# Kernel optimization log

Measured on AMD Instinct MI355X. Metric: run time of the kernel, lower is better.

Reference implementation:

```python
import jax, jax.numpy as jnp
import numpy as np

IN_DIM = 512
REDUCED = IN_DIM // 8  # reduction_ratio = 8
B, C, H, W = 8, 32, 64, IN_DIM


def setup_inputs() -> dict:
    key = jax.random.key(0)
    ks = jax.random.split(key, 9)
    s_in = 1.0 / np.sqrt(IN_DIM)
    inp = {
        "x": jax.random.normal(ks[0], (B, C, H, W), dtype=jnp.float32),
        # torch Linear weights stored here as [in, out] for y = x @ w + b
        "wq": jax.random.uniform(ks[1], (IN_DIM, REDUCED), jnp.float32, -s_in, s_in),
        "bq": jax.random.uniform(ks[2], (REDUCED,), jnp.float32, -s_in, s_in),
        "wk": jax.random.uniform(ks[3], (IN_DIM, REDUCED), jnp.float32, -s_in, s_in),
        "bk": jax.random.uniform(ks[4], (REDUCED,), jnp.float32, -s_in, s_in),
        "wv": jax.random.uniform(ks[5], (IN_DIM, IN_DIM), jnp.float32, -s_in, s_in),
        "bv": jax.random.uniform(ks[6], (IN_DIM,), jnp.float32, -s_in, s_in),
        "wo": jax.random.uniform(ks[7], (IN_DIM, IN_DIM), jnp.float32, -s_in, s_in),
        "bo": jax.random.uniform(ks[8], (IN_DIM,), jnp.float32, -s_in, s_in),
    }
    return inp


def reference(x, wq, bq, wk, bk, wv, bv, wo, bo):
    b, c, h, w = x.shape
    n = c * h  # attention tokens = flattened C*H positions, feature dim = W
    q = (x @ wq + bq).reshape(b, n, REDUCED)   # [B, N, r]
    k = (x @ wk + bk).reshape(b, n, REDUCED)   # [B, N, r]
    v = (x @ wv + bv).reshape(b, n, w)         # [B, N, W]
    energy = jnp.einsum("bnr,bmr->bnm", q, k)  # [B, N, N]
    attn = jax.nn.softmax(energy, axis=-1)
    out = jnp.einsum("bnm,bmd->bnd", attn, v).reshape(b, c, h, w)
    out = out @ wo + bo
    return out + x
```

## Files before the change

### kernel.cpp

```cpp
#include <hip/hip_runtime.h>

typedef __bf16 bf16x8 __attribute__((ext_vector_type(8)));
typedef float  f32x4  __attribute__((ext_vector_type(4)));

union U8 { uint4 v; unsigned short u[8]; };

static __device__ __forceinline__ float bf2f(unsigned short u) {
    union { unsigned int i; float f; } c; c.i = ((unsigned int)u) << 16; return c.f;
}
static __device__ __forceinline__ unsigned short f2bf(float f) {
    union { float f; unsigned int i; } c; c.f = f;
    unsigned int x = c.i;
    unsigned int r = (x + 0x7FFFu + ((x >> 16) & 1u)) >> 16;
    return (unsigned short)r;
}

static __device__ __forceinline__ U8 load8(const float* p) {
    U8 r;
    const float4 a = *(const float4*)p;
    const float4 b = *(const float4*)(p + 4);
    r.u[0] = f2bf(a.x); r.u[1] = f2bf(a.y); r.u[2] = f2bf(a.z); r.u[3] = f2bf(a.w);
    r.u[4] = f2bf(b.x); r.u[5] = f2bf(b.y); r.u[6] = f2bf(b.z); r.u[7] = f2bf(b.w);
    return r;
}

static __device__ __forceinline__ void gld_lds16(const void* g, void* l) {
    __builtin_amdgcn_global_load_lds(
        (const __attribute__((address_space(1))) unsigned int*)g,
        (__attribute__((address_space(3))) unsigned int*)l, 16, 0, 0);
}

__global__ __launch_bounds__(256)
void pack(const float* __restrict__ x, unsigned short* __restrict__ xb,
          const float* __restrict__ bq, const float* __restrict__ bk,
          const float* __restrict__ bv, float* __restrict__ ball,
          const float* __restrict__ wv, const float* __restrict__ wo,
          const float* __restrict__ wq, const float* __restrict__ wk,
          unsigned short* __restrict__ wAllT, unsigned short* __restrict__ woT)
{
    const int bid = blockIdx.x, t = threadIdx.x;
    if (bid < 2048) {
        const long i = ((long)bid * 256 + t) * 16;
        U8 a = load8(x + i);
        U8 b = load8(x + i + 8);
        *(uint4*)(xb + i) = a.v;
        *(uint4*)(xb + i + 8) = b.v;
        if (bid == 0) {
            ball[t]       = t < 64 ? bq[t] : (t < 128 ? bk[t - 64] : bv[t - 128]);
            ball[t + 256] = bv[t + 128];
            if (t < 128) ball[t + 512] = bv[t + 384];
        }
        return;
    }
    __shared__ float sT[64][65];
    const int b2 = bid - 2048;
    const int zz = b2 >> 6, rem = b2 & 63;
    const int cx = rem & 7, ry = rem >> 3;
    const float* src; unsigned short* dst; int C;
    if      (zz == 0) { src = wv; dst = wAllT + 128 * 512; C = 512; }
    else if (zz == 1) { src = wo; dst = woT;               C = 512; }
    else if (zz == 2) { src = wq; dst = wAllT;             C = 64;  }
    else              { src = wk; dst = wAllT + 64 * 512;  C = 64;  }
    const int R = 512;
    const int c0 = cx * 64, r0 = ry * 64;
    if (c0 >= C) return;
    #pragma unroll
    for (int k = 0; k < 16; ++k) {
        const int lin = k * 256 + t;
        const int i = lin >> 6, j = lin & 63;
        sT[i][j] = src[(long)(r0 + i) * C + c0 + j];
    }
    __syncthreads();
    #pragma unroll
    for (int k = 0; k < 16; ++k) {
        const int lin = k * 256 + t;
        const int o = lin >> 6, i2 = lin & 63;
        dst[(long)(c0 + o) * R + r0 + i2] = f2bf(sT[i2][o]);
    }
}

template<bool BIAS, bool RES, bool OUT_F32, bool TRANSC, bool MIXED>
__global__ __launch_bounds__(256, 4)
void gemm128(const unsigned short* __restrict__ A, int lda,
             const unsigned short* __restrict__ B, int ldb,
             void* __restrict__ Cp, int ldc,
             void* __restrict__ Cp2,
             const float* __restrict__ bias,
             const float* __restrict__ resid,
             int K)
{
    __shared__ __align__(16) unsigned short sA[128 * 64];
    __shared__ __align__(16) unsigned short sB[128 * 64];

    const int t = threadIdx.x, wave = t >> 6, lane = t & 63;
    const int lr = lane & 15, quad = lane >> 4;
    const int rowBase = blockIdx.y * 128, colBase = blockIdx.x * 128;
    const int wm = (wave >> 1) * 64, wn = (wave & 1) * 64;

    const int srow  = lane >> 3;
    const int sslot = lane & 7;

    f32x4 acc[4][4];
    #pragma unroll
    for (int mt = 0; mt < 4; ++mt)
        #pragma unroll
        for (int nt = 0; nt < 4; ++nt) acc[mt][nt] = (f32x4){0.f, 0.f, 0.f, 0.f};

    for (int kt = 0; kt < K; kt += 64) {
        #pragma unroll
        for (int is = 0; is < 4; ++is) {
            const int r0  = wave * 32 + is * 8;
            const int row = r0 + srow;
            const int swz = (sslot ^ (row & 7)) << 4;
            gld_lds16((const char*)A + ((long)(rowBase + row) * lda + kt) * 2 + swz,
                      (char*)sA + r0 * 128);
            gld_lds16((const char*)B + ((long)(colBase + row) * ldb + kt) * 2 + swz,
                      (char*)sB + r0 * 128);
        }
        __syncthreads();

        #pragma unroll
        for (int ks = 0; ks < 2; ++ks) {
            const int kb = ks * 64 + quad * 16;
            bf16x8 bfr[4];
            #pragma unroll
            for (int nt = 0; nt < 4; ++nt) {
                const int row = wn + nt * 16 + lr;
                bfr[nt] = *(const bf16x8*)((const char*)sB + row * 128 + (kb ^ ((row & 7) << 4)));
            }
            #pragma unroll
            for (int mt = 0; mt < 4; ++mt) {
                const int row = wm + mt * 16 + lr;
                bf16x8 af = *(const bf16x8*)((const char*)sA + row * 128 + (kb ^ ((row & 7) << 4)));
                #pragma unroll
                for (int nt = 0; nt < 4; ++nt)
                    acc[mt][nt] = __builtin_amdgcn_mfma_f32_16x16x32_bf16(af, bfr[nt], acc[mt][nt], 0, 0, 0);
            }
        }
        __syncthreads();
    }

    float* Cf = (float*)Cp;
    unsigned short* Cb = (unsigned short*)Cp;
    unsigned short* C2 = (unsigned short*)Cp2;
    #pragma unroll
    for (int mt = 0; mt < 4; ++mt)
        #pragma unroll
        for (int nt = 0; nt < 4; ++nt) {
            const int row0 = rowBase + wm + mt * 16 + quad * 4;
            const int col  = colBase + wn + nt * 16 + lr;
            const float b = BIAS ? bias[col] : 0.f;
            if (MIXED && colBase >= 128) {
                const int bat = row0 >> 11, key = row0 & 2047;
                ushort4 v4;
                v4.x = f2bf(acc[mt][nt][0] + b);
                v4.y = f2bf(acc[mt][nt][1] + b);
                v4.z = f2bf(acc[mt][nt][2] + b);
                v4.w = f2bf(acc[mt][nt][3] + b);
                *(ushort4*)&C2[((long)bat * 512 + (col - 128)) * 2048 + key] = v4;
            } else if (TRANSC) {
                const int bat = row0 >> 11, key = row0 & 2047;
                ushort4 v4;
                v4.x = f2bf(acc[mt][nt][0] + b);
                v4.y = f2bf(acc[mt][nt][1] + b);
                v4.z = f2bf(acc[mt][nt][2] + b);
                v4.w = f2bf(acc[mt][nt][3] + b);
                *(ushort4*)&C2[((long)bat * 512 + col) * 2048 + key] = v4;
            } else {
                #pragma unroll
                for (int r = 0; r < 4; ++r) {
                    const int row = row0 + r;
                    float v = acc[mt][nt][r] + b;
                    if (RES)     v += resid[(long)row * ldc + col];
                    if (OUT_F32) Cf[(long)row * ldc + col] = v;
                    else         Cb[(long)row * ldc + col] = f2bf(v);
                }
            }
        }
}

__global__ __launch_bounds__(256, 4)
void flash_attn(const unsigned short* __restrict__ QK,
                const unsigned short* __restrict__ VT,
                unsigned short* __restrict__ O)
{
    __shared__ __align__(16) unsigned short sK[2][64 * 64];
    __shared__ __align__(16) unsigned short sP[2][64 * 72];
    __shared__ float sL[64];

    const int bid = blockIdx.x;
    const int z  = bid & 7;
    const int rr = bid >> 3;
    const int cs = rr & 3;
    const int qt = rr >> 2;

    const int t = threadIdx.x, wave = t >> 6, lane = t & 63;
    const int lr = lane & 15, quad = lane >> 4;

    const long qrow0 = (long)z * 2048 + qt * 64;
    const unsigned short* qp = QK + (qrow0 + wave * 16 + lr) * 128 + quad * 8;
    const bf16x8 qa0 = *(const bf16x8*)(qp);
    const bf16x8 qa1 = *(const bf16x8*)(qp + 32);

    const char* Kb = (const char*)(QK + (long)z * 2048 * 128 + 64);
    const unsigned short* Vb = VT + (long)z * 512 * 2048
                                  + ((long)cs * 128 + wave * 32) * 2048;

    const long stg_go = (long)(wave * 16 + (lane >> 3)) * 256
                      + (((lane & 7) ^ (lane >> 3)) << 4);
    const int swq = (lr & 7) << 4;

    f32x4 acc[4][2];
    #pragma unroll
    for (int mt = 0; mt < 4; ++mt)
        #pragma unroll
        for (int nt = 0; nt < 2; ++nt) acc[mt][nt] = (f32x4){0.f, 0.f, 0.f, 0.f};
    float lsum[4] = {0.f, 0.f, 0.f, 0.f};

    {
        const char* gk = Kb + stg_go;
        char* lk = (char*)sK[0] + wave * 2048;
        gld_lds16(gk, lk);
        gld_lds16(gk + 2048, lk + 1024);
    }
    __syncthreads();

    int cur = 0;
    for (int kt = 0; kt < 32; ++kt) {
        const int key0 = kt * 64;

        bf16x8 vv[2][2];
        #pragma unroll
        for (int nt = 0; nt < 2; ++nt) {
            const unsigned short* vp = Vb + (long)(nt * 16 + lr) * 2048 + key0 + quad * 8;
            vv[nt][0] = *(const bf16x8*)(vp);
            vv[nt][1] = *(const bf16x8*)(vp + 32);
        }

        if (kt < 31) {
            const char* gk = Kb + (long)(kt + 1) * 16384 + stg_go;
            char* lk = (char*)sK[cur ^ 1] + wave * 2048;
            gld_lds16(gk, lk);
            gld_lds16(gk + 2048, lk + 1024);
        }

        const char* sKc = (const char*)sK[cur];
        __bf16* sPb = (__bf16*)sP[cur];
        #pragma unroll
        for (int nt = 0; nt < 4; ++nt) {
            const int kb = (nt * 16 + lr) * 128;
            bf16x8 k0 = *(const bf16x8*)(sKc + kb + ((quad * 16) ^ swq));
            bf16x8 k1 = *(const bf16x8*)(sKc + kb + ((quad * 16 + 64) ^ swq));
            f32x4 sv = (f32x4){0.f, 0.f, 0.f, 0.f};
            sv = __builtin_amdgcn_mfma_f32_16x16x32_bf16(qa0, k0, sv, 0, 0, 0);
            sv = __builtin_amdgcn_mfma_f32_16x16x32_bf16(qa1, k1, sv, 0, 0, 0);
            #pragma unroll
            for (int r = 0; r < 4; ++r) {
                const float e = __expf(sv[r]);
                const __bf16 pb = (__bf16)e;
                lsum[r] += (float)pb;
                sPb[(wave * 16 + quad * 4 + r) * 72 + nt * 16 + lr] = pb;
            }
        }

        __syncthreads();

        const unsigned short* sPc = sP[cur];
        __builtin_amdgcn_s_setprio(1);
        #pragma unroll
        for (int mt = 0; mt < 4; ++mt) {
            const unsigned short* pp = &sPc[(mt * 16 + lr) * 72 + quad * 8];
            bf16x8 p0 = *(const bf16x8*)(pp);
            bf16x8 p1 = *(const bf16x8*)(pp + 32);
            acc[mt][0] = __builtin_amdgcn_mfma_f32_16x16x32_bf16(p0, vv[0][0], acc[mt][0], 0, 0, 0);
            acc[mt][0] = __builtin_amdgcn_mfma_f32_16x16x32_bf16(p1, vv[0][1], acc[mt][0], 0, 0, 0);
            acc[mt][1] = __builtin_amdgcn_mfma_f32_16x16x32_bf16(p0, vv[1][0], acc[mt][1], 0, 0, 0);
            acc[mt][1] = __builtin_amdgcn_mfma_f32_16x16x32_bf16(p1, vv[1][1], acc[mt][1], 0, 0, 0);
        }
        __builtin_amdgcn_s_setprio(0);
        cur ^= 1;
    }

    #pragma unroll
    for (int r = 0; r < 4; ++r) {
        float v = lsum[r];
        v += __shfl_xor(v, 1); v += __shfl_xor(v, 2);
        v += __shfl_xor(v, 4); v += __shfl_xor(v, 8);
        lsum[r] = v;
    }
    if (lr == 0) {
        #pragma unroll
        for (int r = 0; r < 4; ++r) sL[wave * 16 + quad * 4 + r] = lsum[r];
    }
    __syncthreads();

    #pragma unroll
    for (int mt = 0; mt < 4; ++mt) {
        float inv[4];
        #pragma unroll
        for (int r = 0; r < 4; ++r) inv[r] = 1.0f / sL[mt * 16 + quad * 4 + r];
        #pragma unroll
        for (int nt = 0; nt < 2; ++nt) {
            const int col = cs * 128 + wave * 32 + nt * 16 + lr;
            #pragma unroll
            for (int r = 0; r < 4; ++r) {
                const long row = qrow0 + mt * 16 + quad * 4 + r;
                O[row * 512 + col] = f2bf(acc[mt][nt][r] * inv[r]);
            }
        }
    }
}

extern "C" void kernel_launch(void* const* d_in, const int* in_sizes, int n_in,
                              void* d_out, int out_size, void* d_ws, size_t ws_size,
                              hipStream_t stream)
{
    const float* x  = (const float*)d_in[0];
    const float* wq = (const float*)d_in[1];
    const float* bq = (const float*)d_in[2];
    const float* wk = (const float*)d_in[3];
    const float* bk = (const float*)d_in[4];
    const float* wv = (const float*)d_in[5];
    const float* bv = (const float*)d_in[6];
    const float* wo = (const float*)d_in[7];
    const float* bo = (const float*)d_in[8];

    const int W = 512;
    float* out = (float*)d_out;
    dim3 blk(256);
    char* ws = (char*)d_ws;

    const size_t NEED = 56ull << 20;
    if (ws_size < NEED) return;

    unsigned short* QK    = (unsigned short*)(ws);
    unsigned short* VT    = (unsigned short*)(ws + ( 4ull << 20));
    unsigned short* O     = (unsigned short*)(ws + (20ull << 20));
    unsigned short* xb    = (unsigned short*)(ws + (36ull << 20));
    unsigned short* wAllT = (unsigned short*)(ws + (52ull << 20));
    unsigned short* woT   = (unsigned short*)(ws + (53ull << 20));
    float*          ball  = (float*)         (ws + (53ull << 20) + (512ull << 10));

    pack<<<dim3(2048 + 256), blk, 0, stream>>>(x, xb, bq, bk, bv, ball,
                                               wv, wo, wq, wk, wAllT, woT);

    gemm128<true, false, false, false, true><<<dim3(5, 128), blk, 0, stream>>>(
        xb, W, wAllT, W, QK, 128, VT, ball, nullptr, W);

    flash_attn<<<dim3(1024), blk, 0, stream>>>(QK, VT, O);

    gemm128<true, true, true, false, false><<<dim3(4, 128), blk, 0, stream>>>(
        O, W, woT, W, out, W, nullptr, bo, x, W);
}
```

Before: 219.3 us.

## Shrink GEMM row tile to 64 and stage transposed V stores through LDS

The projection and output GEMMs move from 128x128 to 64x128 tiles. That doubles the grid from 640/512 blocks to 1280/1024 and cuts accumulator registers per wave, giving better occupancy and CU fill. The transposed V epilogue now writes bf16 results into an LDS tile and then emits coalesced 16-byte stores along the key dimension, replacing scattered 8-byte stores. The trade-off is less operand reuse per block and an extra barrier in the epilogue.

```diff
diff --git a/kernel.cpp b/kernel.cpp
--- a/kernel.cpp
+++ b/kernel.cpp
@@ -79,42 +79,46 @@
     }
 }
 
-template<bool BIAS, bool RES, bool OUT_F32, bool TRANSC, bool MIXED>
+template<bool BIAS, bool RES, bool OUT_F32, bool MIXED>
 __global__ __launch_bounds__(256, 4)
-void gemm128(const unsigned short* __restrict__ A, int lda,
-             const unsigned short* __restrict__ B, int ldb,
-             void* __restrict__ Cp, int ldc,
-             void* __restrict__ Cp2,
-             const float* __restrict__ bias,
-             const float* __restrict__ resid,
-             int K)
+void gemm64(const unsigned short* __restrict__ A, int lda,
+            const unsigned short* __restrict__ B, int ldb,
+            void* __restrict__ Cp, int ldc,
+            void* __restrict__ Cp2,
+            const float* __restrict__ bias,
+            const float* __restrict__ resid,
+            int K)
 {
-    __shared__ __align__(16) unsigned short sA[128 * 64];
-    __shared__ __align__(16) unsigned short sB[128 * 64];
+    __shared__ __align__(16) unsigned short sMem[12288];
+    unsigned short* sA = sMem;
+    unsigned short* sB = sMem + 4096;
 
     const int t = threadIdx.x, wave = t >> 6, lane = t & 63;
     const int lr = lane & 15, quad = lane >> 4;
-    const int rowBase = blockIdx.y * 128, colBase = blockIdx.x * 128;
-    const int wm = (wave >> 1) * 64, wn = (wave & 1) * 64;
+    const int rowBase = blockIdx.y * 64, colBase = blockIdx.x * 128;
+    const int wm = (wave & 1) * 32, wn = (wave >> 1) * 64;
 
     const int srow  = lane >> 3;
     const int sslot = lane & 7;
-
-    f32x4 acc[4][4];
-    #pragma unroll
-    for (int mt = 0; mt < 4; ++mt)
+    const int swz   = (sslot ^ srow) << 4;
+
+    f32x4 acc[2][4];
+    #pragma unroll
+    for (int mt = 0; mt < 2; ++mt)
         #pragma unroll
         for (int nt = 0; nt < 4; ++nt) acc[mt][nt] = (f32x4){0.f, 0.f, 0.f, 0.f};
 
     for (int kt = 0; kt < K; kt += 64) {
         #pragma unroll
+        for (int is = 0; is < 2; ++is) {
+            const int r0 = wave * 16 + is * 8;
+            gld_lds16((const char*)A + ((long)(rowBase + r0 + srow) * lda + kt) * 2 + swz,
+                      (char*)sA + r0 * 128);
+        }
+        #pragma unroll
         for (int is = 0; is < 4; ++is) {
-            const int r0  = wave * 32 + is * 8;
-            const int row = r0 + srow;
-            const int swz = (sslot ^ (row & 7)) << 4;
-            gld_lds16((const char*)A + ((long)(rowBase + row) * lda + kt) * 2 + swz,
-                      (char*)sA + r0 * 128);
-            gld_lds16((const char*)B + ((long)(colBase + row) * ldb + kt) * 2 + swz,
+            const int r0 = wave * 32 + is * 8;
+            gld_lds16((const char*)B + ((long)(colBase + r0 + srow) * ldb + kt) * 2 + swz,
                       (char*)sB + r0 * 128);
         }
         __syncthreads();
@@ -129,7 +133,7 @@
                 bfr[nt] = *(const bf16x8*)((const char*)sB + row * 128 + (kb ^ ((row & 7) << 4)));
             }
             #pragma unroll
-            for (int mt = 0; mt < 4; ++mt) {
+            for (int mt = 0; mt < 2; ++mt) {
                 const int row = wm + mt * 16 + lr;
                 bf16x8 af = *(const bf16x8*)((const char*)sA + row * 128 + (kb ^ ((row & 7) << 4)));
                 #pragma unroll
@@ -140,41 +144,52 @@
         __syncthreads();
     }
 
-    float* Cf = (float*)Cp;
-    unsigned short* Cb = (unsigned short*)Cp;
-    unsigned short* C2 = (unsigned short*)Cp2;
-    #pragma unroll
-    for (int mt = 0; mt < 4; ++mt)
-        #pragma unroll
-        for (int nt = 0; nt < 4; ++nt) {
-            const int row0 = rowBase + wm + mt * 16 + quad * 4;
-            const int col  = colBase + wn + nt * 16 + lr;
-            const float b = BIAS ? bias[col] : 0.f;
-            if (MIXED && colBase >= 128) {
-                const int bat = row0 >> 11, key = row0 & 2047;
+    if (MIXED && colBase >= 128) {
+        unsigned short* sT = sMem;
+        #pragma unroll
+        for (int mt = 0; mt < 2; ++mt)
+            #pragma unroll
+            for (int nt = 0; nt < 4; ++nt) {
+                const int row0 = wm + mt * 16 + quad * 4;
+                const int col  = wn + nt * 16 + lr;
+                const float b = BIAS ? bias[colBase + col] : 0.f;
                 ushort4 v4;
                 v4.x = f2bf(acc[mt][nt][0] + b);
                 v4.y = f2bf(acc[mt][nt][1] + b);
                 v4.z = f2bf(acc[mt][nt][2] + b);
                 v4.w = f2bf(acc[mt][nt][3] + b);
-                *(ushort4*)&C2[((long)bat * 512 + (col - 128)) * 2048 + key] = v4;
-            } else if (TRANSC) {
-                const int bat = row0 >> 11, key = row0 & 2047;
-                ushort4 v4;
-                v4.x = f2bf(acc[mt][nt][0] + b);
-                v4.y = f2bf(acc[mt][nt][1] + b);
-                v4.z = f2bf(acc[mt][nt][2] + b);
-                v4.w = f2bf(acc[mt][nt][3] + b);
-                *(ushort4*)&C2[((long)bat * 512 + col) * 2048 + key] = v4;
-            } else {
-                #pragma unroll
-                for (int r = 0; r < 4; ++r) {
-                    const int row = row0 + r;
-                    float v = acc[mt][nt][r] + b;
-                    if (RES)     v += resid[(long)row * ldc + col];
-                    if (OUT_F32) Cf[(long)row * ldc + col] = v;
-                    else         Cb[(long)row * ldc + col] = f2bf(v);
-                }
+                *(ushort4*)&sT[col * 72 + row0] = v4;
+            }
+        __syncthreads();
+        unsigned short* C2 = (unsigned short*)Cp2;
+        const int bat = rowBase >> 11, key0 = rowBase & 2047;
+        const long vcol0 = colBase - 128;
+        #pragma unroll
+        for (int ro = 0; ro < 4; ++ro) {
+            const int flat = ro * 256 + t;
+            const int col = flat >> 3, ch = flat & 7;
+            const uint4 v = *(const uint4*)&sT[col * 72 + ch * 8];
+            *(uint4*)&C2[((long)bat * 512 + vcol0 + col) * 2048 + key0 + ch * 8] = v;
+        }
+        return;
+    }
+
+    float* Cf = (float*)Cp;
+    unsigned short* Cb = (unsigned short*)Cp;
+    #pragma unroll
+    for (int mt = 0; mt < 2; ++mt)
+        #pragma unroll
+        for (int nt = 0; nt < 4; ++nt) {
+            const int row0 = rowBase + wm + mt * 16 + quad * 4;
+            const int col  = colBase + wn + nt * 16 + lr;
+            const float b = BIAS ? bias[col] : 0.f;
+            #pragma unroll
+            for (int r = 0; r < 4; ++r) {
+                const int row = row0 + r;
+                float v = acc[mt][nt][r] + b;
+                if (RES)     v += resid[(long)row * ldc + col];
+                if (OUT_F32) Cf[(long)row * ldc + col] = v;
+                else         Cb[(long)row * ldc + col] = f2bf(v);
             }
         }
 }
@@ -344,11 +359,11 @@
     pack<<<dim3(2048 + 256), blk, 0, stream>>>(x, xb, bq, bk, bv, ball,
                                                wv, wo, wq, wk, wAllT, woT);
 
-    gemm128<true, false, false, false, true><<<dim3(5, 128), blk, 0, stream>>>(
+    gemm64<true, false, false, true><<<dim3(5, 256), blk, 0, stream>>>(
         xb, W, wAllT, W, QK, 128, VT, ball, nullptr, W);
 
     flash_attn<<<dim3(1024), blk, 0, stream>>>(QK, VT, O);
 
-    gemm128<true, true, true, false, false><<<dim3(4, 128), blk, 0, stream>>>(
+    gemm64<true, true, true, false><<<dim3(4, 256), blk, 0, stream>>>(
         O, W, woT, W, out, W, nullptr, bo, x, W);
 }
```

Measured after the change: 219.2 us. About the same (-0.1%).
